# Kernel optimization log

Measured on AMD Instinct MI355X. Metric: run time of the kernel, lower is better.

## Reference

```python
import jax, jax.numpy as jnp
import numpy as np

PAD = 3            # ConstantPad1d padding
PAD_VAL = -1.0     # ConstantPad1d value
STRIDE = 1
POOL = 2           # pool_size == pool_stride == 2
BN_EPS = 1e-5


def setup_inputs() -> dict:
    key = jax.random.key(0)
    k1, k2 = jax.random.split(key)
    x = jax.random.normal(k1, (256, 64, 4096), dtype=jnp.float32)
    W = jax.random.normal(k2, (128, 64, 7), dtype=jnp.float32)
    alpha = jnp.ones((1,), dtype=jnp.float32) * 0.25   # nn.PReLU default init
    gamma = jnp.ones((128,), dtype=jnp.float32)
    beta = jnp.zeros((128,), dtype=jnp.float32)
    return {"x": x, "W": W, "alpha": alpha, "gamma": gamma, "beta": beta}


def reference(x, W, alpha, gamma, beta):
    # 1) constant pad with value PAD_VAL along length
    xp = jnp.pad(x, ((0, 0), (0, 0), (PAD, PAD)), constant_values=PAD_VAL)
    # 2) binarize activations and weights (sign; sign(0)=0 as in torch)
    ba = jnp.sign(xp)
    bw = jnp.sign(W)
    # 3) float conv1d on +/-1 values, no bias  -> [B, Cout, L]
    y = jax.lax.conv_general_dilated(
        ba, bw, window_strides=(STRIDE,), padding='VALID',
        dimension_numbers=('NCW', 'OIW', 'NCW'))
    # 4) max pool k=2, s=2 (non-overlapping -> reshape trick)
    B, C, L = y.shape
    y = y[:, :, : (L // POOL) * POOL].reshape(B, C, L // POOL, POOL).max(axis=-1)
    # 5) PReLU with single shared alpha
    y = jnp.where(y > 0, y, alpha[0] * y)
    # 6) BatchNorm1d in training mode: batch stats over (B, L), biased variance
    mean = jnp.mean(y, axis=(0, 2), keepdims=True)
    var = jnp.mean((y - mean) ** 2, axis=(0, 2), keepdims=True)
    y = (y - mean) * jax.lax.rsqrt(var + BN_EPS)
    y = y * gamma[None, :, None] + beta[None, :, None]
    return y
```

## Files before the change

### kernel.cpp

```cpp
#include <hip/hip_runtime.h>
#include <stdint.h>

#define BATCH 256
#define CIN   64
#define LIN   4096
#define PADN  3
#define LPAD  (LIN + 2*PADN)
#define COUT  128
#define KW    7
#define LPOOL 2048
#define NPERCH (256LL * 2048LL)

typedef unsigned long long u64;

__global__ __launch_bounds__(256) void pack_x_kernel(const float* __restrict__ x,
                                                     ulonglong2* __restrict__ px)
{
    int pos = blockIdx.x * 256 + threadIdx.x;
    int b   = blockIdx.y;
    if (pos >= LPAD) return;
    u64 s = 0, z = 0;
    int lx = pos - PADN;
    if (lx < 0 || lx >= LIN) {
        s = 0;
        z = ~0ull;
    } else {
        const float* xb = x + (size_t)b * CIN * LIN + lx;
        #pragma unroll
        for (int c = 0; c < CIN; ++c) {
            float v = xb[(size_t)c * LIN];
            s |= ((u64)(v > 0.0f))  << c;
            z |= ((u64)(v != 0.0f)) << c;
        }
    }
    px[(size_t)b * LPAD + pos] = make_ulonglong2(s, z);
}

__global__ void pack_w_kernel(const float* __restrict__ w,
                              ulonglong2* __restrict__ pw,
                              unsigned int* __restrict__ wflag)
{
    int t = blockIdx.x * blockDim.x + threadIdx.x;
    if (t >= COUT * KW) return;
    int co = t / KW, k = t % KW;
    u64 s = 0, z = 0;
    for (int c = 0; c < CIN; ++c) {
        float v = w[((size_t)co * CIN + c) * KW + k];
        s |= ((u64)(v > 0.0f))  << c;
        z |= ((u64)(v != 0.0f)) << c;
    }
    pw[t] = make_ulonglong2(s, z);
    if (z != ~0ull) atomicOr(wflag, 1u);
}

__device__ __forceinline__ int conv_pooled(const ulonglong2 w8[8],
                                           const ulonglong2* __restrict__ wj,
                                           bool fast)
{
    if (fast) {
        int c0 = 0, c1 = 0;
        #pragma unroll
        for (int k = 0; k < KW; ++k) {
            u64 wsk = wj[k].x;
            c0 += __popcll(w8[k].x     ^ wsk);
            c1 += __popcll(w8[k + 1].x ^ wsk);
        }
        int m = (c0 < c1) ? c0 : c1;
        return (CIN * KW) - 2 * m;
    } else {
        int d0 = 0, d1 = 0;
        #pragma unroll
        for (int k = 0; k < KW; ++k) {
            u64 wsk = wj[k].x, wzk = wj[k].y;
            u64 m0 = w8[k].y     & wzk;
            u64 m1 = w8[k + 1].y & wzk;
            d0 += __popcll(m0) - 2 * __popcll((w8[k].x     ^ wsk) & m0);
            d1 += __popcll(m1) - 2 * __popcll((w8[k + 1].x ^ wsk) & m1);
        }
        return (d0 > d1) ? d0 : d1;
    }
}

__global__ __launch_bounds__(256) void conv_stats_kernel(
    const ulonglong2* __restrict__ px, const ulonglong2* __restrict__ pw,
    const unsigned int* __restrict__ wflag, unsigned long long* __restrict__ stats)
{
    const int tid = threadIdx.x;
    const int co0 = blockIdx.x * 4;
    const int b   = blockIdx.y;
    const bool wbad = (*wflag != 0);

    int sp[4] = {0,0,0,0}, sn[4] = {0,0,0,0}, qp[4] = {0,0,0,0}, qn[4] = {0,0,0,0};

    for (int i = 0; i < 8; ++i) {
        int lp = i * 256 + tid;
        const ulonglong2* xw = px + (size_t)b * LPAD + 2 * lp;
        ulonglong2 w8[8];
        #pragma unroll
        for (int t = 0; t < 8; ++t) w8[t] = xw[t];
        u64 zand = w8[0].y & w8[1].y & w8[2].y & w8[3].y &
                   w8[4].y & w8[5].y & w8[6].y & w8[7].y;
        bool fast = (zand == ~0ull) && !wbad;
        #pragma unroll
        for (int j = 0; j < 4; ++j) {
            int p = conv_pooled(w8, pw + (size_t)(co0 + j) * KW, fast);
            if (p > 0) { sp[j] += p; qp[j] += p * p; }
            else       { sn[j] += p; qn[j] += p * p; }
        }
    }

    int vals[16];
    #pragma unroll
    for (int j = 0; j < 4; ++j) {
        vals[j*4+0] = sp[j]; vals[j*4+1] = sn[j];
        vals[j*4+2] = qp[j]; vals[j*4+3] = qn[j];
    }
    #pragma unroll
    for (int v = 0; v < 16; ++v)
        for (int off = 32; off >= 1; off >>= 1)
            vals[v] += __shfl_down(vals[v], off, 64);

    __shared__ int redu[4][16];
    int wid = tid >> 6, lane = tid & 63;
    if (lane == 0) {
        #pragma unroll
        for (int v = 0; v < 16; ++v) redu[wid][v] = vals[v];
    }
    __syncthreads();
    if (tid < 16) {
        int s = redu[0][tid] + redu[1][tid] + redu[2][tid] + redu[3][tid];
        int j = tid >> 2, si = tid & 3;
        atomicAdd(&stats[(size_t)(co0 + j) * 4 + si],
                  (unsigned long long)(long long)s);
    }
}

__global__ void finalize_kernel(const unsigned long long* __restrict__ stats,
                                const float* __restrict__ alpha,
                                const float* __restrict__ gamma,
                                const float* __restrict__ beta,
                                float2* __restrict__ scsh)
{
    int c = threadIdx.x;
    if (c >= COUT) return;
    long long sp = (long long)stats[c*4+0];
    long long sn = (long long)stats[c*4+1];
    long long qp = (long long)stats[c*4+2];
    long long qn = (long long)stats[c*4+3];
    double a   = (double)alpha[0];
    double N   = (double)NPERCH;
    double sum = (double)sp + a * (double)sn;
    double ssq = (double)qp + a * a * (double)qn;
    double mean = sum / N;
    double var  = ssq / N - mean * mean;
    double inv  = 1.0 / sqrt(var + 1e-5);
    double g    = (double)gamma[c];
    float sc = (float)(g * inv);
    float sh = (float)((double)beta[c] - mean * g * inv);
    scsh[c] = make_float2(sc, sh);
}

__global__ __launch_bounds__(256) void conv_write_kernel(
    const ulonglong2* __restrict__ px, const ulonglong2* __restrict__ pw,
    const unsigned int* __restrict__ wflag, const float2* __restrict__ scsh,
    const float* __restrict__ alpha, float* __restrict__ out)
{
    const int tid = threadIdx.x;
    const int co0 = blockIdx.x * 4;
    const int b   = blockIdx.y;
    const bool wbad = (*wflag != 0);
    const float a = alpha[0];
    float2 ss[4];
    #pragma unroll
    for (int j = 0; j < 4; ++j) ss[j] = scsh[co0 + j];

    for (int i = 0; i < 8; ++i) {
        int lp = i * 256 + tid;
        const ulonglong2* xw = px + (size_t)b * LPAD + 2 * lp;
        ulonglong2 w8[8];
        #pragma unroll
        for (int t = 0; t < 8; ++t) w8[t] = xw[t];
        u64 zand = w8[0].y & w8[1].y & w8[2].y & w8[3].y &
                   w8[4].y & w8[5].y & w8[6].y & w8[7].y;
        bool fast = (zand == ~0ull) && !wbad;
        #pragma unroll
        for (int j = 0; j < 4; ++j) {
            int p = conv_pooled(w8, pw + (size_t)(co0 + j) * KW, fast);
            float yf = (p > 0) ? (float)p : a * (float)p;
            out[((size_t)b * COUT + co0 + j) * LPOOL + lp] = fmaf(yf, ss[j].x, ss[j].y);
        }
    }
}

extern "C" void kernel_launch(void* const* d_in, const int* in_sizes, int n_in,
                              void* d_out, int out_size, void* d_ws, size_t ws_size,
                              hipStream_t stream)
{
    const float* x     = (const float*)d_in[0];
    const float* W     = (const float*)d_in[1];
    const float* alpha = (const float*)d_in[2];
    const float* gamma = (const float*)d_in[3];
    const float* beta  = (const float*)d_in[4];
    float* out = (float*)d_out;

    char* ws = (char*)d_ws;
    size_t off = 0;
    ulonglong2* px = (ulonglong2*)(ws + off); off += (size_t)BATCH * LPAD * sizeof(ulonglong2);
    ulonglong2* pw = (ulonglong2*)(ws + off); off += (size_t)COUT * KW * sizeof(ulonglong2);
    unsigned long long* stats = (unsigned long long*)(ws + off); off += (size_t)COUT * 4 * 8;
    unsigned int* wflag = (unsigned int*)(ws + off); off += 16;
    float2* scsh = (float2*)(ws + off); off += (size_t)COUT * 8;

    hipMemsetAsync(stats, 0, (size_t)COUT * 4 * 8 + 16, stream);

    pack_x_kernel<<<dim3((LPAD + 255) / 256, BATCH), 256, 0, stream>>>(x, px);
    pack_w_kernel<<<dim3(4), 256, 0, stream>>>(W, pw, wflag);
    conv_stats_kernel<<<dim3(COUT / 4, BATCH), 256, 0, stream>>>(px, pw, wflag, stats);
    finalize_kernel<<<dim3(1), 128, 0, stream>>>(stats, alpha, gamma, beta, scsh);
    conv_write_kernel<<<dim3(COUT / 4, BATCH), 256, 0, stream>>>(px, pw, wflag, scsh, alpha, out);
}
```

Measured before the change: 356.3 us.

## Split packed sign/zero planes, stage sign row in LDS, use zero bitmap

Splits the packed activation into separate sign and nonzero planes. Each conv block now stages the batch row's sign words in shared memory and uses a per-position bitmap of nonzero-mask exceptions to pick the fast path, instead of loading both words for every window. Blocks now handle 8 output channels instead of 4, which halves the grid and doubles reuse of the staged row. The costs are an extra atomicOr pass in the pack kernel, more registers per thread, and a serialized slow path that reads the nonzero plane from global memory.

```diff
diff --git a/kernel.cpp b/kernel.cpp
--- a/kernel.cpp
+++ b/kernel.cpp
@@ -9,12 +9,16 @@
 #define COUT  128
 #define KW    7
 #define LPOOL 2048
+#define JCO   8
+#define ZWORDS 65
 #define NPERCH (256LL * 2048LL)
 
 typedef unsigned long long u64;
 
 __global__ __launch_bounds__(256) void pack_x_kernel(const float* __restrict__ x,
-                                                     ulonglong2* __restrict__ px)
+                                                     u64* __restrict__ sx,
+                                                     u64* __restrict__ zx,
+                                                     u64* __restrict__ zbits)
 {
     int pos = blockIdx.x * 256 + threadIdx.x;
     int b   = blockIdx.y;
@@ -33,7 +37,10 @@
             z |= ((u64)(v != 0.0f)) << c;
         }
     }
-    px[(size_t)b * LPAD + pos] = make_ulonglong2(s, z);
+    sx[(size_t)b * LPAD + pos] = s;
+    zx[(size_t)b * LPAD + pos] = z;
+    if (z != ~0ull)
+        atomicOr(&zbits[(size_t)b * ZWORDS + (pos >> 6)], 1ull << (pos & 63));
 }
 
 __global__ void pack_w_kernel(const float* __restrict__ w,
@@ -53,81 +60,125 @@
     if (z != ~0ull) atomicOr(wflag, 1u);
 }
 
-__device__ __forceinline__ int conv_pooled(const ulonglong2 w8[8],
-                                           const ulonglong2* __restrict__ wj,
-                                           bool fast)
-{
-    if (fast) {
-        int c0 = 0, c1 = 0;
-        #pragma unroll
-        for (int k = 0; k < KW; ++k) {
-            u64 wsk = wj[k].x;
-            c0 += __popcll(w8[k].x     ^ wsk);
-            c1 += __popcll(w8[k + 1].x ^ wsk);
-        }
-        int m = (c0 < c1) ? c0 : c1;
-        return (CIN * KW) - 2 * m;
+__device__ __forceinline__ int conv_pooled_exact(const u64 w8s[8],
+                                                 const u64* __restrict__ zrow,
+                                                 int bpos,
+                                                 const ulonglong2* __restrict__ wj)
+{
+    u64 w8z[8];
+    #pragma unroll
+    for (int t = 0; t < 8; ++t) w8z[t] = zrow[bpos + t];
+    int d0 = 0, d1 = 0;
+    #pragma unroll
+    for (int k = 0; k < KW; ++k) {
+        u64 wsk = wj[k].x, wzk = wj[k].y;
+        u64 m0 = w8z[k]     & wzk;
+        u64 m1 = w8z[k + 1] & wzk;
+        d0 += __popcll(m0) - 2 * __popcll((w8s[k]     ^ wsk) & m0);
+        d1 += __popcll(m1) - 2 * __popcll((w8s[k + 1] ^ wsk) & m1);
+    }
+    return (d0 > d1) ? d0 : d1;
+}
+
+__device__ __forceinline__ void conv_group(const u64* __restrict__ sxs,
+                                           const u64* __restrict__ zbs,
+                                           const u64* __restrict__ zrow,
+                                           const ulonglong2* __restrict__ pw,
+                                           int co0, int lp, unsigned wbad,
+                                           int p[JCO])
+{
+    const int bpos = 2 * lp;
+    u64 w8[8];
+    const u64* wp = sxs + bpos;
+    #pragma unroll
+    for (int t = 0; t < 8; ++t) w8[t] = wp[t];
+
+    int wi = bpos >> 6, sh = bpos & 63;
+    u64 zlo = zbs[wi], zhi = zbs[wi + 1];
+    unsigned zm = (unsigned)(((zlo >> sh) | ((zhi << 1) << (63 - sh))) & 0xFFull);
+
+    if ((zm | wbad) == 0) {
+        #pragma unroll
+        for (int j = 0; j < JCO; ++j) {
+            const ulonglong2* wj = pw + (size_t)(co0 + j) * KW;
+            int c0 = 0, c1 = 0;
+            #pragma unroll
+            for (int k = 0; k < KW; ++k) {
+                u64 wsk = wj[k].x;
+                c0 += __popcll(w8[k]     ^ wsk);
+                c1 += __popcll(w8[k + 1] ^ wsk);
+            }
+            int m = (c0 < c1) ? c0 : c1;
+            p[j] = (CIN * KW) - 2 * m;
+        }
     } else {
-        int d0 = 0, d1 = 0;
-        #pragma unroll
-        for (int k = 0; k < KW; ++k) {
-            u64 wsk = wj[k].x, wzk = wj[k].y;
-            u64 m0 = w8[k].y     & wzk;
-            u64 m1 = w8[k + 1].y & wzk;
-            d0 += __popcll(m0) - 2 * __popcll((w8[k].x     ^ wsk) & m0);
-            d1 += __popcll(m1) - 2 * __popcll((w8[k + 1].x ^ wsk) & m1);
-        }
-        return (d0 > d1) ? d0 : d1;
+        #pragma unroll 1
+        for (int j = 0; j < JCO; ++j)
+            p[j] = conv_pooled_exact(w8, zrow, bpos, pw + (size_t)(co0 + j) * KW);
     }
 }
 
 __global__ __launch_bounds__(256) void conv_stats_kernel(
-    const ulonglong2* __restrict__ px, const ulonglong2* __restrict__ pw,
+    const u64* __restrict__ sx, const u64* __restrict__ zx,
+    const u64* __restrict__ zbits, const ulonglong2* __restrict__ pw,
     const unsigned int* __restrict__ wflag, unsigned long long* __restrict__ stats)
 {
+    __shared__ __align__(16) u64 sxs[LPAD];
+    __shared__ u64 zbs[ZWORDS + 1];
+    __shared__ int redu[4][32];
+
     const int tid = threadIdx.x;
-    const int co0 = blockIdx.x * 4;
+    const int co0 = blockIdx.x * JCO;
     const int b   = blockIdx.y;
-    const bool wbad = (*wflag != 0);
-
-    int sp[4] = {0,0,0,0}, sn[4] = {0,0,0,0}, qp[4] = {0,0,0,0}, qn[4] = {0,0,0,0};
+    const unsigned wbad = *wflag;
+
+    const u64* srow = sx + (size_t)b * LPAD;
+    for (int i = tid; i < LPAD; i += 256) sxs[i] = srow[i];
+    if (tid < ZWORDS) zbs[tid] = zbits[(size_t)b * ZWORDS + tid];
+    if (tid == ZWORDS) zbs[ZWORDS] = 0;
+    __syncthreads();
+
+    const u64* zrow = zx + (size_t)b * LPAD;
+
+    int sp[JCO], sn[JCO], qp[JCO], qn[JCO];
+    #pragma unroll
+    for (int j = 0; j < JCO; ++j) { sp[j]=0; sn[j]=0; qp[j]=0; qn[j]=0; }
 
     for (int i = 0; i < 8; ++i) {
         int lp = i * 256 + tid;
-        const ulonglong2* xw = px + (size_t)b * LPAD + 2 * lp;
-        ulonglong2 w8[8];
-        #pragma unroll
-        for (int t = 0; t < 8; ++t) w8[t] = xw[t];
-        u64 zand = w8[0].y & w8[1].y & w8[2].y & w8[3].y &
-                   w8[4].y & w8[5].y & w8[6].y & w8[7].y;
-        bool fast = (zand == ~0ull) && !wbad;
-        #pragma unroll
-        for (int j = 0; j < 4; ++j) {
-            int p = conv_pooled(w8, pw + (size_t)(co0 + j) * KW, fast);
-            if (p > 0) { sp[j] += p; qp[j] += p * p; }
-            else       { sn[j] += p; qn[j] += p * p; }
-        }
-    }
-
-    int vals[16];
-    #pragma unroll
-    for (int j = 0; j < 4; ++j) {
+        int p[JCO];
+        conv_group(sxs, zbs, zrow, pw, co0, lp, wbad, p);
+        #pragma unroll
+        for (int j = 0; j < JCO; ++j) {
+            int pp = p[j];
+            bool pos = pp > 0;
+            int p2 = pp * pp;
+            sp[j] += pos ? pp : 0;
+            sn[j] += pos ? 0  : pp;
+            qp[j] += pos ? p2 : 0;
+            qn[j] += pos ? 0  : p2;
+        }
+    }
+
+    int vals[32];
+    #pragma unroll
+    for (int j = 0; j < JCO; ++j) {
         vals[j*4+0] = sp[j]; vals[j*4+1] = sn[j];
         vals[j*4+2] = qp[j]; vals[j*4+3] = qn[j];
     }
     #pragma unroll
-    for (int v = 0; v < 16; ++v)
+    for (int v = 0; v < 32; ++v)
+        #pragma unroll
         for (int off = 32; off >= 1; off >>= 1)
             vals[v] += __shfl_down(vals[v], off, 64);
 
-    __shared__ int redu[4][16];
     int wid = tid >> 6, lane = tid & 63;
     if (lane == 0) {
         #pragma unroll
-        for (int v = 0; v < 16; ++v) redu[wid][v] = vals[v];
+        for (int v = 0; v < 32; ++v) redu[wid][v] = vals[v];
     }
     __syncthreads();
-    if (tid < 16) {
+    if (tid < 32) {
         int s = redu[0][tid] + redu[1][tid] + redu[2][tid] + redu[3][tid];
         int j = tid >> 2, si = tid & 3;
         atomicAdd(&stats[(size_t)(co0 + j) * 4 + si],
@@ -155,39 +206,47 @@
     double var  = ssq / N - mean * mean;
     double inv  = 1.0 / sqrt(var + 1e-5);
     double g    = (double)gamma[c];
-    float sc = (float)(g * inv);
-    float sh = (float)((double)beta[c] - mean * g * inv);
-    scsh[c] = make_float2(sc, sh);
+    scsh[c] = make_float2((float)(g * inv),
+                          (float)((double)beta[c] - mean * g * inv));
 }
 
 __global__ __launch_bounds__(256) void conv_write_kernel(
-    const ulonglong2* __restrict__ px, const ulonglong2* __restrict__ pw,
+    const u64* __restrict__ sx, const u64* __restrict__ zx,
+    const u64* __restrict__ zbits, const ulonglong2* __restrict__ pw,
     const unsigned int* __restrict__ wflag, const float2* __restrict__ scsh,
     const float* __restrict__ alpha, float* __restrict__ out)
 {
+    __shared__ __align__(16) u64 sxs[LPAD];
+    __shared__ u64 zbs[ZWORDS + 1];
+
     const int tid = threadIdx.x;
-    const int co0 = blockIdx.x * 4;
+    const int co0 = blockIdx.x * JCO;
     const int b   = blockIdx.y;
-    const bool wbad = (*wflag != 0);
+    const unsigned wbad = *wflag;
     const float a = alpha[0];
-    float2 ss[4];
-    #pragma unroll
-    for (int j = 0; j < 4; ++j) ss[j] = scsh[co0 + j];
+
+    const u64* srow = sx + (size_t)b * LPAD;
+    for (int i = tid; i < LPAD; i += 256) sxs[i] = srow[i];
+    if (tid < ZWORDS) zbs[tid] = zbits[(size_t)b * ZWORDS + tid];
+    if (tid == ZWORDS) zbs[ZWORDS] = 0;
+    __syncthreads();
+
+    const u64* zrow = zx + (size_t)b * LPAD;
+
+    float2 ss[JCO];
+    #pragma unroll
+    for (int j = 0; j < JCO; ++j) ss[j] = scsh[co0 + j];
 
     for (int i = 0; i < 8; ++i) {
         int lp = i * 256 + tid;
-        const ulonglong2* xw = px + (size_t)b * LPAD + 2 * lp;
-        ulonglong2 w8[8];
-        #pragma unroll
-        for (int t = 0; t < 8; ++t) w8[t] = xw[t];
-        u64 zand = w8[0].y & w8[1].y & w8[2].y & w8[3].y &
-                   w8[4].y & w8[5].y & w8[6].y & w8[7].y;
-        bool fast = (zand == ~0ull) && !wbad;
-        #pragma unroll
-        for (int j = 0; j < 4; ++j) {
-            int p = conv_pooled(w8, pw + (size_t)(co0 + j) * KW, fast);
-            float yf = (p > 0) ? (float)p : a * (float)p;
-            out[((size_t)b * COUT + co0 + j) * LPOOL + lp] = fmaf(yf, ss[j].x, ss[j].y);
+        int p[JCO];
+        conv_group(sxs, zbs, zrow, pw, co0, lp, wbad, p);
+        #pragma unroll
+        for (int j = 0; j < JCO; ++j) {
+            int pp = p[j];
+            float yf = (pp > 0) ? (float)pp : a * (float)pp;
+            out[((size_t)b * COUT + co0 + j) * LPOOL + lp] =
+                fmaf(yf, ss[j].x, ss[j].y);
         }
     }
 }
@@ -205,17 +264,20 @@
 
     char* ws = (char*)d_ws;
     size_t off = 0;
-    ulonglong2* px = (ulonglong2*)(ws + off); off += (size_t)BATCH * LPAD * sizeof(ulonglong2);
-    ulonglong2* pw = (ulonglong2*)(ws + off); off += (size_t)COUT * KW * sizeof(ulonglong2);
-    unsigned long long* stats = (unsigned long long*)(ws + off); off += (size_t)COUT * 4 * 8;
+    u64* sxw = (u64*)(ws + off);        off += (size_t)BATCH * LPAD * 8;
+    u64* zxw = (u64*)(ws + off);        off += (size_t)BATCH * LPAD * 8;
+    ulonglong2* pw = (ulonglong2*)(ws + off); off += (size_t)COUT * KW * 16;
+    float2* scsh = (float2*)(ws + off); off += (size_t)COUT * 8;
+    unsigned long long* stats = (unsigned long long*)(ws + off);
+    size_t zoff = off;                  off += (size_t)COUT * 4 * 8;
     unsigned int* wflag = (unsigned int*)(ws + off); off += 16;
-    float2* scsh = (float2*)(ws + off); off += (size_t)COUT * 8;
-
-    hipMemsetAsync(stats, 0, (size_t)COUT * 4 * 8 + 16, stream);
-
-    pack_x_kernel<<<dim3((LPAD + 255) / 256, BATCH), 256, 0, stream>>>(x, px);
+    u64* zbits = (u64*)(ws + off);      off += (size_t)BATCH * ZWORDS * 8;
+
+    hipMemsetAsync(ws + zoff, 0, off - zoff, stream);
+
+    pack_x_kernel<<<dim3((LPAD + 255) / 256, BATCH), 256, 0, stream>>>(x, sxw, zxw, zbits);
     pack_w_kernel<<<dim3(4), 256, 0, stream>>>(W, pw, wflag);
-    conv_stats_kernel<<<dim3(COUT / 4, BATCH), 256, 0, stream>>>(px, pw, wflag, stats);
+    conv_stats_kernel<<<dim3(COUT / JCO, BATCH), 256, 0, stream>>>(sxw, zxw, zbits, pw, wflag, stats);
     finalize_kernel<<<dim3(1), 128, 0, stream>>>(stats, alpha, gamma, beta, scsh);
-    conv_write_kernel<<<dim3(COUT / 4, BATCH), 256, 0, stream>>>(px, pw, wflag, scsh, alpha, out);
-}
+    conv_write_kernel<<<dim3(COUT / JCO, BATCH), 256, 0, stream>>>(sxw, zxw, zbits, pw, wflag, scsh, alpha, out);
+}
```

Result: slower. 374.4 us (+5.1%).

## Compute binary conv with int8 MFMA instead of popcount bitpacking

Applied to the files above, without the earlier changes.

Replaces the bit-packed XOR/popcount convolution with an int8 layout (sign values -1/0/+1, 64 channels per position) fed to 32x32x32 int8 MFMA instructions, with weights held in registers and max-pool done on accumulator pairs. Stats atomics are spread across 64 batch buckets to reduce contention, and the workspace may be chunked over the batch if it is too small. The int8 layout makes the packed input 4x larger than the bitpacked one, trading more memory traffic for matrix-core throughput and removing the zero-handling slow path.

```diff
diff --git a/kernel.cpp b/kernel.cpp
--- a/kernel.cpp
+++ b/kernel.cpp
@@ -5,137 +5,149 @@
 #define CIN   64
 #define LIN   4096
 #define PADN  3
-#define LPAD  (LIN + 2*PADN)
+#define LPAD  4102
 #define COUT  128
 #define KW    7
 #define LPOOL 2048
+#define NBUCKET 64
 #define NPERCH (256LL * 2048LL)
 
 typedef unsigned long long u64;
+typedef __attribute__((ext_vector_type(4)))  int i32x4;
+typedef __attribute__((ext_vector_type(16))) int i32x16;
+
+#define ACC_ZERO {0,0,0,0,0,0,0,0,0,0,0,0,0,0,0,0}
 
 __global__ __launch_bounds__(256) void pack_x_kernel(const float* __restrict__ x,
-                                                     ulonglong2* __restrict__ px)
-{
-    int pos = blockIdx.x * 256 + threadIdx.x;
-    int b   = blockIdx.y;
-    if (pos >= LPAD) return;
-    u64 s = 0, z = 0;
-    int lx = pos - PADN;
-    if (lx < 0 || lx >= LIN) {
-        s = 0;
-        z = ~0ull;
-    } else {
-        const float* xb = x + (size_t)b * CIN * LIN + lx;
-        #pragma unroll
-        for (int c = 0; c < CIN; ++c) {
-            float v = xb[(size_t)c * LIN];
-            s |= ((u64)(v > 0.0f))  << c;
-            z |= ((u64)(v != 0.0f)) << c;
-        }
-    }
-    px[(size_t)b * LPAD + pos] = make_ulonglong2(s, z);
-}
-
-__global__ void pack_w_kernel(const float* __restrict__ w,
-                              ulonglong2* __restrict__ pw,
-                              unsigned int* __restrict__ wflag)
-{
-    int t = blockIdx.x * blockDim.x + threadIdx.x;
-    if (t >= COUT * KW) return;
-    int co = t / KW, k = t % KW;
-    u64 s = 0, z = 0;
-    for (int c = 0; c < CIN; ++c) {
-        float v = w[((size_t)co * CIN + c) * KW + k];
-        s |= ((u64)(v > 0.0f))  << c;
-        z |= ((u64)(v != 0.0f)) << c;
-    }
-    pw[t] = make_ulonglong2(s, z);
-    if (z != ~0ull) atomicOr(wflag, 1u);
-}
-
-__device__ __forceinline__ int conv_pooled(const ulonglong2 w8[8],
-                                           const ulonglong2* __restrict__ wj,
-                                           bool fast)
-{
-    if (fast) {
-        int c0 = 0, c1 = 0;
-        #pragma unroll
-        for (int k = 0; k < KW; ++k) {
-            u64 wsk = wj[k].x;
-            c0 += __popcll(w8[k].x     ^ wsk);
-            c1 += __popcll(w8[k + 1].x ^ wsk);
-        }
-        int m = (c0 < c1) ? c0 : c1;
-        return (CIN * KW) - 2 * m;
-    } else {
-        int d0 = 0, d1 = 0;
-        #pragma unroll
-        for (int k = 0; k < KW; ++k) {
-            u64 wsk = wj[k].x, wzk = wj[k].y;
-            u64 m0 = w8[k].y     & wzk;
-            u64 m1 = w8[k + 1].y & wzk;
-            d0 += __popcll(m0) - 2 * __popcll((w8[k].x     ^ wsk) & m0);
-            d1 += __popcll(m1) - 2 * __popcll((w8[k + 1].x ^ wsk) & m1);
-        }
-        return (d0 > d1) ? d0 : d1;
-    }
-}
-
-__global__ __launch_bounds__(256) void conv_stats_kernel(
-    const ulonglong2* __restrict__ px, const ulonglong2* __restrict__ pw,
-    const unsigned int* __restrict__ wflag, unsigned long long* __restrict__ stats)
-{
-    const int tid = threadIdx.x;
-    const int co0 = blockIdx.x * 4;
-    const int b   = blockIdx.y;
-    const bool wbad = (*wflag != 0);
-
-    int sp[4] = {0,0,0,0}, sn[4] = {0,0,0,0}, qp[4] = {0,0,0,0}, qn[4] = {0,0,0,0};
-
-    for (int i = 0; i < 8; ++i) {
-        int lp = i * 256 + tid;
-        const ulonglong2* xw = px + (size_t)b * LPAD + 2 * lp;
-        ulonglong2 w8[8];
-        #pragma unroll
-        for (int t = 0; t < 8; ++t) w8[t] = xw[t];
-        u64 zand = w8[0].y & w8[1].y & w8[2].y & w8[3].y &
-                   w8[4].y & w8[5].y & w8[6].y & w8[7].y;
-        bool fast = (zand == ~0ull) && !wbad;
+                                                     char* __restrict__ sx,
+                                                     int b_base)
+{
+    const int t  = threadIdx.x;
+    const int lt = blockIdx.x;
+    const int bl = blockIdx.y;
+    const int b  = b_base + bl;
+    const int l  = lt * 256 + t;
+    const float* xb = x + (size_t)b * CIN * LIN + l;
+
+    int o[16];
+    #pragma unroll
+    for (int cw = 0; cw < 16; ++cw) {
+        unsigned wv = 0;
         #pragma unroll
         for (int j = 0; j < 4; ++j) {
-            int p = conv_pooled(w8, pw + (size_t)(co0 + j) * KW, fast);
-            if (p > 0) { sp[j] += p; qp[j] += p * p; }
-            else       { sn[j] += p; qn[j] += p * p; }
-        }
-    }
-
-    int vals[16];
+            float v = xb[(size_t)(cw * 4 + j) * LIN];
+            unsigned s = (v > 0.0f) ? 1u : ((v < 0.0f) ? 0xFFu : 0u);
+            wv |= s << (8 * j);
+        }
+        o[cw] = (int)wv;
+    }
+    i32x4* dst = (i32x4*)(sx + ((size_t)bl * LPAD + (l + PADN)) * 64);
+    dst[0] = (i32x4){o[0],  o[1],  o[2],  o[3]};
+    dst[1] = (i32x4){o[4],  o[5],  o[6],  o[7]};
+    dst[2] = (i32x4){o[8],  o[9],  o[10], o[11]};
+    dst[3] = (i32x4){o[12], o[13], o[14], o[15]};
+
+    const i32x4 ff = (i32x4){-1, -1, -1, -1};
+    if (lt == 0 && t < PADN) {
+        i32x4* pd = (i32x4*)(sx + ((size_t)bl * LPAD + t) * 64);
+        pd[0] = ff; pd[1] = ff; pd[2] = ff; pd[3] = ff;
+    }
+    if (lt == 15 && t < PADN) {
+        i32x4* pd = (i32x4*)(sx + ((size_t)bl * LPAD + (LIN + PADN) + t) * 64);
+        pd[0] = ff; pd[1] = ff; pd[2] = ff; pd[3] = ff;
+    }
+}
+
+__global__ __launch_bounds__(256) void pack_w_kernel(const float* __restrict__ w,
+                                                     char* __restrict__ pwb)
+{
+    int idx = blockIdx.x * 256 + threadIdx.x;
+    if (idx >= KW * COUT * CIN) return;
+    int kk = idx >> 13;
+    int co = (idx >> 6) & 127;
+    int c  = idx & 63;
+    float v = w[((size_t)co * CIN + c) * KW + kk];
+    pwb[idx] = (char)((v > 0.0f) ? 1 : ((v < 0.0f) ? -1 : 0));
+}
+
+
+__global__ __launch_bounds__(256, 2) void conv_stats_kernel(
+    const char* __restrict__ sx, const char* __restrict__ pwb,
+    u64* __restrict__ stats, int b_base)
+{
+    const int tid  = threadIdx.x;
+    const int lane = tid & 63;
+    const int w    = tid >> 6;
+    const int ngrp = w & 1;
+    const int mgrp = w >> 1;
+    const int col  = lane & 31;
+    const int hi   = lane >> 5;
+    const int bl   = blockIdx.y;
+    const int mchunk = blockIdx.x;
+
+    i32x4 bf[KW][2][2];
     #pragma unroll
-    for (int j = 0; j < 4; ++j) {
-        vals[j*4+0] = sp[j]; vals[j*4+1] = sn[j];
-        vals[j*4+2] = qp[j]; vals[j*4+3] = qn[j];
-    }
-    #pragma unroll
-    for (int v = 0; v < 16; ++v)
-        for (int off = 32; off >= 1; off >>= 1)
-            vals[v] += __shfl_down(vals[v], off, 64);
-
-    __shared__ int redu[4][16];
-    int wid = tid >> 6, lane = tid & 63;
-    if (lane == 0) {
-        #pragma unroll
-        for (int v = 0; v < 16; ++v) redu[wid][v] = vals[v];
-    }
-    __syncthreads();
-    if (tid < 16) {
-        int s = redu[0][tid] + redu[1][tid] + redu[2][tid] + redu[3][tid];
-        int j = tid >> 2, si = tid & 3;
-        atomicAdd(&stats[(size_t)(co0 + j) * 4 + si],
-                  (unsigned long long)(long long)s);
-    }
-}
-
-__global__ void finalize_kernel(const unsigned long long* __restrict__ stats,
+    for (int kk = 0; kk < KW; ++kk)
+        #pragma unroll
+        for (int kb = 0; kb < 2; ++kb)
+            #pragma unroll
+            for (int n = 0; n < 2; ++n)
+                bf[kk][kb][n] = *(const i32x4*)(pwb +
+                    (size_t)((kk * COUT + ngrp * 64 + n * 32 + col) * 64
+                             + kb * 32 + hi * 16));
+
+    const char* sxb = sx + (size_t)bl * LPAD * 64;
+    int sp0=0, sn0=0, qp0=0, qn0=0, sp1=0, sn1=0, qp1=0, qn1=0;
+
+    for (int mt = 0; mt < 4; ++mt) {
+        const int q0 = mchunk * 256 + mgrp * 128 + mt * 32;
+        i32x16 acc0 = ACC_ZERO, acc1 = ACC_ZERO;
+        #pragma unroll
+        for (int kk = 0; kk < KW; ++kk) {
+            const char* ar = sxb + (size_t)(q0 + col + kk) * 64;
+            i32x4 a0 = *(const i32x4*)(ar + hi * 16);
+            i32x4 a1 = *(const i32x4*)(ar + 32 + hi * 16);
+            acc0 = __builtin_amdgcn_mfma_i32_32x32x32_i8(a0, bf[kk][0][0], acc0, 0, 0, 0);
+            acc0 = __builtin_amdgcn_mfma_i32_32x32x32_i8(a1, bf[kk][1][0], acc0, 0, 0, 0);
+            acc1 = __builtin_amdgcn_mfma_i32_32x32x32_i8(a0, bf[kk][0][1], acc1, 0, 0, 0);
+            acc1 = __builtin_amdgcn_mfma_i32_32x32x32_i8(a1, bf[kk][1][1], acc1, 0, 0, 0);
+        }
+        #pragma unroll
+        for (int r = 0; r < 8; ++r) {
+            int p = acc0[2*r] > acc0[2*r+1] ? acc0[2*r] : acc0[2*r+1];
+            int q = p * p;
+            bool pos = p > 0;
+            sp0 += pos ? p : 0;  sn0 += pos ? 0 : p;
+            qp0 += pos ? q : 0;  qn0 += pos ? 0 : q;
+            p = acc1[2*r] > acc1[2*r+1] ? acc1[2*r] : acc1[2*r+1];
+            q = p * p;
+            pos = p > 0;
+            sp1 += pos ? p : 0;  sn1 += pos ? 0 : p;
+            qp1 += pos ? q : 0;  qn1 += pos ? 0 : q;
+        }
+    }
+
+    sp0 += __shfl_xor(sp0, 32);  sn0 += __shfl_xor(sn0, 32);
+    qp0 += __shfl_xor(qp0, 32);  qn0 += __shfl_xor(qn0, 32);
+    sp1 += __shfl_xor(sp1, 32);  sn1 += __shfl_xor(sn1, 32);
+    qp1 += __shfl_xor(qp1, 32);  qn1 += __shfl_xor(qn1, 32);
+
+    if (hi == 0) {
+        const int bkt = (b_base + bl) & (NBUCKET - 1);
+        u64* s0 = stats + (size_t)(bkt * COUT + ngrp * 64 + col) * 4;
+        atomicAdd(&s0[0], (u64)(long long)sp0);
+        atomicAdd(&s0[1], (u64)(long long)sn0);
+        atomicAdd(&s0[2], (u64)(long long)qp0);
+        atomicAdd(&s0[3], (u64)(long long)qn0);
+        u64* s1 = stats + (size_t)(bkt * COUT + ngrp * 64 + 32 + col) * 4;
+        atomicAdd(&s1[0], (u64)(long long)sp1);
+        atomicAdd(&s1[1], (u64)(long long)sn1);
+        atomicAdd(&s1[2], (u64)(long long)qp1);
+        atomicAdd(&s1[3], (u64)(long long)qn1);
+    }
+}
+
+__global__ void finalize_kernel(const u64* __restrict__ stats,
                                 const float* __restrict__ alpha,
                                 const float* __restrict__ gamma,
                                 const float* __restrict__ beta,
@@ -143,51 +155,80 @@
 {
     int c = threadIdx.x;
     if (c >= COUT) return;
-    long long sp = (long long)stats[c*4+0];
-    long long sn = (long long)stats[c*4+1];
-    long long qp = (long long)stats[c*4+2];
-    long long qn = (long long)stats[c*4+3];
-    double a   = (double)alpha[0];
-    double N   = (double)NPERCH;
-    double sum = (double)sp + a * (double)sn;
-    double ssq = (double)qp + a * a * (double)qn;
+    long long s[4] = {0, 0, 0, 0};
+    for (int bk = 0; bk < NBUCKET; ++bk)
+        #pragma unroll
+        for (int i = 0; i < 4; ++i)
+            s[i] += (long long)stats[(size_t)(bk * COUT + c) * 4 + i];
+    double a    = (double)alpha[0];
+    double N    = (double)NPERCH;
+    double sum  = (double)s[0] + a * (double)s[1];
+    double ssq  = (double)s[2] + a * a * (double)s[3];
     double mean = sum / N;
     double var  = ssq / N - mean * mean;
     double inv  = 1.0 / sqrt(var + 1e-5);
     double g    = (double)gamma[c];
-    float sc = (float)(g * inv);
-    float sh = (float)((double)beta[c] - mean * g * inv);
-    scsh[c] = make_float2(sc, sh);
-}
-
-__global__ __launch_bounds__(256) void conv_write_kernel(
-    const ulonglong2* __restrict__ px, const ulonglong2* __restrict__ pw,
-    const unsigned int* __restrict__ wflag, const float2* __restrict__ scsh,
-    const float* __restrict__ alpha, float* __restrict__ out)
-{
-    const int tid = threadIdx.x;
-    const int co0 = blockIdx.x * 4;
-    const int b   = blockIdx.y;
-    const bool wbad = (*wflag != 0);
+    scsh[c] = make_float2((float)(g * inv),
+                          (float)((double)beta[c] - mean * g * inv));
+}
+
+__global__ __launch_bounds__(256, 2) void conv_write_kernel(
+    const char* __restrict__ sx, const char* __restrict__ pwb,
+    const float2* __restrict__ scsh, const float* __restrict__ alpha,
+    float* __restrict__ out, int b_base)
+{
+    const int tid  = threadIdx.x;
+    const int lane = tid & 63;
+    const int w    = tid >> 6;
+    const int ngrp = w & 1;
+    const int mgrp = w >> 1;
+    const int col  = lane & 31;
+    const int hi   = lane >> 5;
+    const int bl   = blockIdx.y;
+    const int mchunk = blockIdx.x;
+
+    i32x4 bf[KW][2][2];
+    #pragma unroll
+    for (int kk = 0; kk < KW; ++kk)
+        #pragma unroll
+        for (int kb = 0; kb < 2; ++kb)
+            #pragma unroll
+            for (int n = 0; n < 2; ++n)
+                bf[kk][kb][n] = *(const i32x4*)(pwb +
+                    (size_t)((kk * COUT + ngrp * 64 + n * 32 + col) * 64
+                             + kb * 32 + hi * 16));
+
+    const char* sxb = sx + (size_t)bl * LPAD * 64;
     const float a = alpha[0];
-    float2 ss[4];
-    #pragma unroll
-    for (int j = 0; j < 4; ++j) ss[j] = scsh[co0 + j];
-
-    for (int i = 0; i < 8; ++i) {
-        int lp = i * 256 + tid;
-        const ulonglong2* xw = px + (size_t)b * LPAD + 2 * lp;
-        ulonglong2 w8[8];
-        #pragma unroll
-        for (int t = 0; t < 8; ++t) w8[t] = xw[t];
-        u64 zand = w8[0].y & w8[1].y & w8[2].y & w8[3].y &
-                   w8[4].y & w8[5].y & w8[6].y & w8[7].y;
-        bool fast = (zand == ~0ull) && !wbad;
-        #pragma unroll
-        for (int j = 0; j < 4; ++j) {
-            int p = conv_pooled(w8, pw + (size_t)(co0 + j) * KW, fast);
-            float yf = (p > 0) ? (float)p : a * (float)p;
-            out[((size_t)b * COUT + co0 + j) * LPOOL + lp] = fmaf(yf, ss[j].x, ss[j].y);
+    const float2 ss0 = scsh[ngrp * 64 + col];
+    const float2 ss1 = scsh[ngrp * 64 + 32 + col];
+    const int gb = b_base + bl;
+    float* orow0 = out + ((size_t)gb * COUT + ngrp * 64 + col) * LPOOL;
+    float* orow1 = orow0 + (size_t)32 * LPOOL;
+
+    for (int mt = 0; mt < 4; ++mt) {
+        const int q0 = mchunk * 256 + mgrp * 128 + mt * 32;
+        i32x16 acc0 = ACC_ZERO, acc1 = ACC_ZERO;
+        #pragma unroll
+        for (int kk = 0; kk < KW; ++kk) {
+            const char* ar = sxb + (size_t)(q0 + col + kk) * 64;
+            i32x4 a0 = *(const i32x4*)(ar + hi * 16);
+            i32x4 a1 = *(const i32x4*)(ar + 32 + hi * 16);
+            acc0 = __builtin_amdgcn_mfma_i32_32x32x32_i8(a0, bf[kk][0][0], acc0, 0, 0, 0);
+            acc0 = __builtin_amdgcn_mfma_i32_32x32x32_i8(a1, bf[kk][1][0], acc0, 0, 0, 0);
+            acc1 = __builtin_amdgcn_mfma_i32_32x32x32_i8(a0, bf[kk][0][1], acc1, 0, 0, 0);
+            acc1 = __builtin_amdgcn_mfma_i32_32x32x32_i8(a1, bf[kk][1][1], acc1, 0, 0, 0);
+        }
+        const int lp0 = q0 >> 1;
+        #pragma unroll
+        for (int r = 0; r < 8; ++r) {
+            const int prow = (r & 1) + 4 * (r >> 1) + 2 * hi;
+            int p = acc0[2*r] > acc0[2*r+1] ? acc0[2*r] : acc0[2*r+1];
+            float y = (p > 0) ? (float)p : a * (float)p;
+            orow0[lp0 + prow] = fmaf(y, ss0.x, ss0.y);
+            p = acc1[2*r] > acc1[2*r+1] ? acc1[2*r] : acc1[2*r+1];
+            y = (p > 0) ? (float)p : a * (float)p;
+            orow1[lp0 + prow] = fmaf(y, ss1.x, ss1.y);
         }
     }
 }
@@ -203,19 +244,44 @@
     const float* beta  = (const float*)d_in[4];
     float* out = (float*)d_out;
 
+    const size_t PER_B    = (size_t)LPAD * 64;
+    const size_t pwb_sz   = (size_t)KW * COUT * CIN;
+    const size_t stats_sz = (size_t)NBUCKET * COUT * 4 * 8;
+    const size_t scsh_sz  = (size_t)COUT * 8;
+    const size_t fixed    = pwb_sz + stats_sz + scsh_sz + 1024;
+
+    int nb = BATCH;
+    if (ws_size < PER_B * BATCH + fixed) {
+        size_t avail = (ws_size > fixed) ? (ws_size - fixed) : PER_B;
+        nb = (int)(avail / PER_B);
+        if (nb < 1) nb = 1;
+        if (nb > BATCH) nb = BATCH;
+    }
+
     char* ws = (char*)d_ws;
-    size_t off = 0;
-    ulonglong2* px = (ulonglong2*)(ws + off); off += (size_t)BATCH * LPAD * sizeof(ulonglong2);
-    ulonglong2* pw = (ulonglong2*)(ws + off); off += (size_t)COUT * KW * sizeof(ulonglong2);
-    unsigned long long* stats = (unsigned long long*)(ws + off); off += (size_t)COUT * 4 * 8;
-    unsigned int* wflag = (unsigned int*)(ws + off); off += 16;
-    float2* scsh = (float2*)(ws + off); off += (size_t)COUT * 8;
-
-    hipMemsetAsync(stats, 0, (size_t)COUT * 4 * 8 + 16, stream);
-
-    pack_x_kernel<<<dim3((LPAD + 255) / 256, BATCH), 256, 0, stream>>>(x, px);
-    pack_w_kernel<<<dim3(4), 256, 0, stream>>>(W, pw, wflag);
-    conv_stats_kernel<<<dim3(COUT / 4, BATCH), 256, 0, stream>>>(px, pw, wflag, stats);
+    char* sx = ws;
+    size_t off = ((PER_B * (size_t)nb) + 255) & ~(size_t)255;
+    char* pwb = ws + off;               off = (off + pwb_sz + 255) & ~(size_t)255;
+    u64* stats = (u64*)(ws + off);      off = (off + stats_sz + 255) & ~(size_t)255;
+    float2* scsh = (float2*)(ws + off);
+
+    hipMemsetAsync(stats, 0, stats_sz, stream);
+    pack_w_kernel<<<dim3(224), 256, 0, stream>>>(W, pwb);
+
+    for (int b0 = 0; b0 < BATCH; b0 += nb) {
+        int n = (BATCH - b0 < nb) ? (BATCH - b0) : nb;
+        pack_x_kernel<<<dim3(16, n), 256, 0, stream>>>(x, sx, b0);
+        conv_stats_kernel<<<dim3(16, n), 256, 0, stream>>>(sx, pwb, stats, b0);
+    }
     finalize_kernel<<<dim3(1), 128, 0, stream>>>(stats, alpha, gamma, beta, scsh);
-    conv_write_kernel<<<dim3(COUT / 4, BATCH), 256, 0, stream>>>(px, pw, wflag, scsh, alpha, out);
-}
+
+    if (nb == BATCH) {
+        conv_write_kernel<<<dim3(16, BATCH), 256, 0, stream>>>(sx, pwb, scsh, alpha, out, 0);
+    } else {
+        for (int b0 = 0; b0 < BATCH; b0 += nb) {
+            int n = (BATCH - b0 < nb) ? (BATCH - b0) : nb;
+            pack_x_kernel<<<dim3(16, n), 256, 0, stream>>>(x, sx, b0);
+            conv_write_kernel<<<dim3(16, n), 256, 0, stream>>>(sx, pwb, scsh, alpha, out, b0);
+        }
+    }
+}
```

Result: slower. 383.1 us (+7.5%).
